# Performance work log

Measured on AMD Instinct MI355X. Metric: run time of the kernel, lower is better.

## Reference

```python
import jax, jax.numpy as jnp
import numpy as np
from jax import lax

EPS = 1e-5  # BatchNorm eps (inference-style BN with running stats)


def _bn(x, g, b, m, v):
    scale = g / jnp.sqrt(v + EPS)
    return x * scale[None, :, None, None] + (b - m * scale)[None, :, None, None]


def _conv1x1_bn(x, w, g, b, m, v):
    # ConvNormActivation(in_ch, out, k=1, activation=None) -> 1x1 conv (no bias) + BN
    y = jnp.einsum('bchw,oc->bohw', x, w)
    return _bn(y, g, b, m, v)


def _upsample_bilinear_ac(x, scale):
    # nn.Upsample(scale_factor=scale, mode='bilinear', align_corners=True)
    B, C, H, W = x.shape
    Ho, Wo = H * scale, W * scale

    def coords(n_in, n_out):
        s = jnp.arange(n_out, dtype=x.dtype) * ((n_in - 1) / (n_out - 1))
        i0 = jnp.clip(jnp.floor(s).astype(jnp.int32), 0, n_in - 2)
        t = s - i0.astype(x.dtype)
        return i0, t

    iy, ty = coords(H, Ho)
    ix, tx = coords(W, Wo)
    x = x[:, :, iy, :] * (1 - ty)[None, None, :, None] + x[:, :, iy + 1, :] * ty[None, None, :, None]
    x = x[:, :, :, ix] * (1 - tx) + x[:, :, :, ix + 1] * tx
    return x


def _dcnv2(x, off_w, off_b, w):
    # DCNv2: internal 3x3 conv -> 18 offsets (dy,dx per tap) + 9 sigmoid masks,
    # then modulated deformable 3x3 conv (stride 1, pad 1, no bias).
    B, C, H, W = x.shape
    K2 = 9
    om = lax.conv_general_dilated(x, off_w, (1, 1), ((1, 1), (1, 1)),
                                  dimension_numbers=('NCHW', 'OIHW', 'NCHW'))
    om = om + off_b[None, :, None, None]
    off = om[:, :2 * K2].reshape(B, K2, 2, H, W)          # (dy, dx) per kernel tap
    mask = jax.nn.sigmoid(om[:, 2 * K2:3 * K2])           # [B,9,H,W]

    ky, kx = jnp.meshgrid(jnp.arange(3), jnp.arange(3), indexing='ij')
    base_y = (jnp.arange(H)[None, :, None] + (ky.reshape(K2) - 1)[:, None, None]).astype(x.dtype)  # [9,H,1]
    base_x = (jnp.arange(W)[None, None, :] + (kx.reshape(K2) - 1)[:, None, None]).astype(x.dtype)  # [9,1,W]
    sy = base_y[None] + off[:, :, 0]                      # [B,9,H,W]
    sx = base_x[None] + off[:, :, 1]

    xf = x.reshape(B, C, H * W)
    y0 = jnp.floor(sy)
    x0 = jnp.floor(sx)
    val = jnp.zeros((B, C, K2, H, W), x.dtype)
    for dy in (0, 1):
        for dx in (0, 1):
            yy = y0 + dy
            xx = x0 + dx
            wgt = (1 - jnp.abs(sy - yy)) * (1 - jnp.abs(sx - xx))
            valid = (yy >= 0) & (yy <= H - 1) & (xx >= 0) & (xx <= W - 1)
            idx = jnp.clip(yy, 0, H - 1).astype(jnp.int32) * W + jnp.clip(xx, 0, W - 1).astype(jnp.int32)
            g = jnp.take_along_axis(xf, idx.reshape(B, 1, -1), axis=2).reshape(B, C, K2, H, W)
            val = val + g * (wgt * valid.astype(x.dtype))[:, None]
    val = val * mask[:, None]
    return jnp.einsum('bckhw,ock->bohw', val, w.reshape(w.shape[0], C, K2))


def _forward(f0, f1, f2, f3,
             w0, g0, b0, m0, v0, w1, g1, b1, m1, v1,
             w2, g2, b2, m2, v2, w3, g3, b3, m3, v3,
             off_w, off_b, dcn_w, gf, bf, mf, vf):
    x1 = _conv1x1_bn(f0, w0, g0, b0, m0, v0)
    x2 = _upsample_bilinear_ac(_conv1x1_bn(f1, w1, g1, b1, m1, v1), 2)
    x3 = _upsample_bilinear_ac(_conv1x1_bn(f2, w2, g2, b2, m2, v2), 4)
    x4 = _upsample_bilinear_ac(_conv1x1_bn(f3, w3, g3, b3, m3, v3), 8)
    x = jax.nn.relu(x1 + x2 + x3 + x4)
    y = _dcnv2(x, off_w, off_b, dcn_w)
    return jax.nn.relu(_bn(y, gf, bf, mf, vf))


def setup_inputs() -> dict:
    key = jax.random.key(0)
    ks = iter(jax.random.split(key, 64))

    def rn(shape, scale=1.0):
        return jax.random.normal(next(ks), shape, dtype=jnp.float32) * scale

    def ru(shape):
        return jax.random.uniform(next(ks), shape, dtype=jnp.float32)

    C = 64
    inp = {}
    inp['f0'] = rn((4, 64, 160, 160))
    inp['f1'] = rn((4, 128, 80, 80))
    inp['f2'] = rn((4, 256, 40, 40))
    inp['f3'] = rn((4, 512, 20, 20))
    for i, cin in enumerate([64, 128, 256, 512]):
        inp[f'w{i}'] = rn((C, cin), 1.0 / np.sqrt(cin))
        inp[f'g{i}'] = rn((C,))
        inp[f'b{i}'] = rn((C,))
        inp[f'm{i}'] = rn((C,))
        inp[f'v{i}'] = ru((C,))
    inp['off_w'] = rn((27, C, 3, 3), 0.01)   # small offsets, like post-training DCN
    inp['off_b'] = rn((27,), 0.01)
    inp['dcn_w'] = rn((C, C, 3, 3), 1.0 / np.sqrt(C * 9))
    inp['gf'] = rn((C,))
    inp['bf'] = rn((C,))
    inp['mf'] = rn((C,))
    inp['vf'] = ru((C,))
    return inp


def reference(f0, f1, f2, f3,
              w0, g0, b0, m0, v0, w1, g1, b1, m1, v1,
              w2, g2, b2, m2, v2, w3, g3, b3, m3, v3,
              off_w, off_b, dcn_w, gf, bf, mf, vf):
    return _forward(f0, f1, f2, f3,
                    w0, g0, b0, m0, v0, w1, g1, b1, m1, v1,
                    w2, g2, b2, m2, v2, w3, g3, b3, m3, v3,
                    off_w, off_b, dcn_w, gf, bf, mf, vf)
```

## Files before the change

kernel.cpp:

```cpp
#include <hip/hip_runtime.h>
#include <math.h>

#define EPSB 1e-5f

constexpr int B_ = 4;
constexpr int C_ = 64;
constexpr int H_ = 160;
constexpr int W_ = 160;
constexpr int HW_ = H_ * W_;

constexpr size_t X_OFF   = 0;
constexpr size_t Y1_OFF  = X_OFF  + (size_t)B_ * HW_ * 64;
constexpr size_t Y2_OFF  = Y1_OFF + (size_t)B_ * 6400 * 64;
constexpr size_t Y3_OFF  = Y2_OFF + (size_t)B_ * 1600 * 64;
constexpr size_t OM_OFF  = Y3_OFF + (size_t)B_ * 400 * 64;
constexpr size_t WR0_OFF = OM_OFF + (size_t)B_ * HW_ * 27;
constexpr size_t WTB_OFF = WR0_OFF + 4096;
constexpr size_t RWB_OFF = WTB_OFF + (9 * 64 * 72) / 2;
constexpr size_t SB_OFF  = RWB_OFF + (9 * 32 * 64) / 2;
constexpr size_t WR1_OFF = X_OFF + 0;
constexpr size_t WR2_OFF = X_OFF + 8192;
constexpr size_t WR3_OFF = X_OFF + 24576;

typedef short bf16x8 __attribute__((ext_vector_type(8)));
typedef float f32x4 __attribute__((ext_vector_type(4)));

static __device__ __forceinline__ unsigned short f2bf(float f) {
    unsigned int u = __float_as_uint(f);
    u += 0x7fff + ((u >> 16) & 1);
    return (unsigned short)(u >> 16);
}

__global__ __launch_bounds__(256) void prep_kernel(
    const float* __restrict__ g0, const float* __restrict__ b0, const float* __restrict__ m0, const float* __restrict__ v0,
    const float* __restrict__ g1, const float* __restrict__ b1, const float* __restrict__ m1, const float* __restrict__ v1,
    const float* __restrict__ g2, const float* __restrict__ b2, const float* __restrict__ m2, const float* __restrict__ v2,
    const float* __restrict__ g3, const float* __restrict__ b3, const float* __restrict__ m3, const float* __restrict__ v3,
    const float* __restrict__ gf, const float* __restrict__ bf, const float* __restrict__ mf, const float* __restrict__ vf,
    const float* __restrict__ w0, const float* __restrict__ w1, const float* __restrict__ w2, const float* __restrict__ w3,
    const float* __restrict__ dcn_w, const float* __restrict__ off_w,
    float* __restrict__ ws)
{
    int tid = blockIdx.x * 256 + threadIdx.x;
    if (tid < 320) {
        int j = tid >> 6, c = tid & 63;
        const float *g, *b, *m, *v;
        switch (j) {
            case 0: g = g0; b = b0; m = m0; v = v0; break;
            case 1: g = g1; b = b1; m = m1; v = v1; break;
            case 2: g = g2; b = b2; m = m2; v = v2; break;
            case 3: g = g3; b = b3; m = m3; v = v3; break;
            default: g = gf; b = bf; m = mf; v = vf; break;
        }
        float sc = g[c] * rsqrtf(v[c] + EPSB);
        ws[SB_OFF + j * 128 + c]      = sc;
        ws[SB_OFF + j * 128 + 64 + c] = b[c] - m[c] * sc;
        return;
    }
    int t = tid - 320;
    if (t < 4096) {
        int ci = t >> 6, o = t & 63;
        ws[WR0_OFF + t] = w0[o * 64 + ci];
        return;
    }
    t -= 4096;
    if (t < 9 * 64 * 72) {
        int k = t / 4608, r = t % 4608, o = r / 72, c = r % 72;
        float v = (c < 64) ? dcn_w[o * 576 + c * 9 + k] : 0.f;
        ((unsigned short*)(ws + WTB_OFF))[t] = f2bf(v);
        return;
    }
    t -= 9 * 64 * 72;
    if (t < 9 * 32 * 64) {
        int tap = t >> 11, r = t & 2047, o = r >> 6, ci = r & 63;
        float v = (o < 27) ? off_w[o * 576 + ci * 9 + tap] : 0.f;
        ((unsigned short*)(ws + RWB_OFF))[t] = f2bf(v);
        return;
    }
    t -= 9 * 32 * 64;
    if (t < 8192) {
        int ci = t >> 6, o = t & 63;
        ws[WR1_OFF + t] = w1[o * 128 + ci];
        return;
    }
    t -= 8192;
    if (t < 16384) {
        int ci = t >> 6, o = t & 63;
        ws[WR2_OFF + t] = w2[o * 256 + ci];
        return;
    }
    t -= 16384;
    if (t < 32768) {
        int ci = t >> 6, o = t & 63;
        ws[WR3_OFF + t] = w3[o * 512 + ci];
        return;
    }
}

__global__ __launch_bounds__(256) void conv1x1_bn_kernel(
    const float* __restrict__ f, const float* __restrict__ wr,
    const float* __restrict__ sb, float* __restrict__ out, int Cin, int hw)
{
    int xcd = blockIdx.x & 7, slot = blockIdx.x >> 3;
    int b = xcd >> 1;
    int g = (xcd & 1) * (hw >> 3) + slot;
    int o = threadIdx.x & 63;
    int p = g * 4 + (threadIdx.x >> 6);
    p = __builtin_amdgcn_readfirstlane(p);
    b = __builtin_amdgcn_readfirstlane(b);
    const float* fb = f + (size_t)b * Cin * hw + p;
    float acc = 0.f;
#pragma unroll 8
    for (int ci = 0; ci < Cin; ++ci) acc = fmaf(fb[(size_t)ci * hw], wr[ci * 64 + o], acc);
    out[((size_t)b * hw + p) * 64 + o] = fmaf(acc, sb[o], sb[64 + o]);
}

__global__ __launch_bounds__(256) void fuse_kernel(const float* __restrict__ f0, float* __restrict__ ws)
{
    __shared__ float Ot[64 * 68];

    int tid = threadIdx.x;
    int blk = blockIdx.x;
    int xcd = blk & 7, slot = blk >> 3;
    int b = xcd >> 1;
    int t = (xcd & 1) * 200 + slot;
    int p0 = t * 64;
    int lane = tid & 63;
    int cb = __builtin_amdgcn_readfirstlane(tid >> 6);
    int p = p0 + lane;
    const float* wr0 = ws + WR0_OFF + cb * 16;
    const float* sb  = ws + SB_OFF;

    {
        float acc[16];
#pragma unroll
        for (int i = 0; i < 16; i++) acc[i] = 0.f;

        const float* f0b = f0 + (size_t)b * 64 * HW_ + p;
        for (int ci0 = 0; ci0 < 64; ci0 += 8) {
            float fv[8];
#pragma unroll
            for (int j = 0; j < 8; j++) fv[j] = f0b[(size_t)(ci0 + j) * HW_];
#pragma unroll
            for (int j = 0; j < 8; j++) {
                const float* wrow = wr0 + (ci0 + j) * 64;
#pragma unroll
                for (int i = 0; i < 16; i++) acc[i] = fmaf(fv[j], wrow[i], acc[i]);
            }
        }
        float* orow = Ot + lane * 68 + cb * 16;
#pragma unroll
        for (int i = 0; i < 16; i++) {
            int o = cb * 16 + i;
            orow[i] = fmaf(acc[i], sb[o], sb[64 + o]);
        }
    }
    __syncthreads();

    {
        int chunk = lane & 15, pxo = lane >> 4;
        float* xb = ws + X_OFF + ((size_t)b * HW_ + p0) * 64;
#pragma unroll
        for (int r = 0; r < 4; r++) {
            int gpx = cb * 16 + r * 4 + pxo;
            int gp = p0 + gpx;
            int h = gp / W_, w = gp % W_;

            float fy1 = h * (79.f / 159.f); int i1 = (int)fy1; if (i1 > 78) i1 = 78; float ty1 = fy1 - i1;
            float fx1 = w * (79.f / 159.f); int j1 = (int)fx1; if (j1 > 78) j1 = 78; float tx1 = fx1 - j1;
            const float* y1 = ws + Y1_OFF + ((size_t)b * 6400 + (size_t)(i1 * 80 + j1)) * 64 + chunk * 4;
            float fy2 = h * (39.f / 159.f); int i2 = (int)fy2; if (i2 > 38) i2 = 38; float ty2 = fy2 - i2;
            float fx2 = w * (39.f / 159.f); int j2 = (int)fx2; if (j2 > 38) j2 = 38; float tx2 = fx2 - j2;
            const float* y2 = ws + Y2_OFF + ((size_t)b * 1600 + (size_t)(i2 * 40 + j2)) * 64 + chunk * 4;
            float fy3 = h * (19.f / 159.f); int i3 = (int)fy3; if (i3 > 18) i3 = 18; float ty3 = fy3 - i3;
            float fx3 = w * (19.f / 159.f); int j3 = (int)fx3; if (j3 > 18) j3 = 18; float tx3 = fx3 - j3;
            const float* y3 = ws + Y3_OFF + ((size_t)b * 400 + (size_t)(i3 * 20 + j3)) * 64 + chunk * 4;

            f32x4 A[12];
            A[0]  = *(const f32x4*)(y1);
            A[1]  = *(const f32x4*)(y1 + 64);
            A[2]  = *(const f32x4*)(y1 + 80 * 64);
            A[3]  = *(const f32x4*)(y1 + 81 * 64);
            A[4]  = *(const f32x4*)(y2);
            A[5]  = *(const f32x4*)(y2 + 64);
            A[6]  = *(const f32x4*)(y2 + 40 * 64);
            A[7]  = *(const f32x4*)(y2 + 41 * 64);
            A[8]  = *(const f32x4*)(y3);
            A[9]  = *(const f32x4*)(y3 + 64);
            A[10] = *(const f32x4*)(y3 + 20 * 64);
            A[11] = *(const f32x4*)(y3 + 21 * 64);

            f32x4 v = *(const f32x4*)(Ot + gpx * 68 + chunk * 4);

            float w00, w01, w10, w11;
            w00 = (1.f - ty1) * (1.f - tx1); w01 = (1.f - ty1) * tx1; w10 = ty1 * (1.f - tx1); w11 = ty1 * tx1;
#pragma unroll
            for (int j = 0; j < 4; j++)
                v[j] += A[0][j] * w00 + A[1][j] * w01 + A[2][j] * w10 + A[3][j] * w11;
            w00 = (1.f - ty2) * (1.f - tx2); w01 = (1.f - ty2) * tx2; w10 = ty2 * (1.f - tx2); w11 = ty2 * tx2;
#pragma unroll
            for (int j = 0; j < 4; j++)
                v[j] += A[4][j] * w00 + A[5][j] * w01 + A[6][j] * w10 + A[7][j] * w11;
            w00 = (1.f - ty3) * (1.f - tx3); w01 = (1.f - ty3) * tx3; w10 = ty3 * (1.f - tx3); w11 = ty3 * tx3;
#pragma unroll
            for (int j = 0; j < 4; j++)
                v[j] += A[8][j] * w00 + A[9][j] * w01 + A[10][j] * w10 + A[11][j] * w11;

#pragma unroll
            for (int j = 0; j < 4; j++) v[j] = fmaxf(v[j], 0.f);
            *(f32x4*)(xb + (size_t)gpx * 64 + chunk * 4) = v;
        }
    }
}

__global__ __launch_bounds__(256, 4) void dcn_fused_kernel(const float* __restrict__ off_b,
                                                           float* __restrict__ ws, float* __restrict__ out)
{
    __shared__ __align__(16) unsigned short A_lds[2][64 * 72];
    __shared__ float OMs[64 * 27];

    int tid = threadIdx.x;
    int blk = blockIdx.x;
    int xcd = blk & 7, slot = blk >> 3;
    int b = xcd >> 1;
    int t = (xcd & 1) * 200 + slot;
    int p0 = t * 64;
    int lane = tid & 63, cb = tid >> 6;
    int px = lane;
    int p = p0 + px;
    int h = p / W_, w = p % W_;
    int mrow = lane & 15, quad = lane >> 4;
    int chunk = lane & 15, pxo = lane >> 4;

    const unsigned short* rwb = (const unsigned short*)(ws + RWB_OFF);
    const unsigned short* wtb = (const unsigned short*)(ws + WTB_OFF);
    const float* xb = ws + X_OFF + (size_t)b * HW_ * 64;
    const float* sb = ws + SB_OFF + 4 * 128;

    {
        f32x4 acc2[2];
        acc2[0] = (f32x4){0.f, 0.f, 0.f, 0.f};
        acc2[1] = (f32x4){0.f, 0.f, 0.f, 0.f};

        for (int kk = 0; kk < 9; kk += 2) {
#pragma unroll
            for (int u = 0; u < 2; u++) {
                int tap = kk + u;
                if (tap > 8) break;
                int dy = tap / 3 - 1, dx = tap % 3 - 1;
                int delta = dy * W_ + dx;
                int  pss[4];
                bool vlds[4];
#pragma unroll
                for (int r = 0; r < 4; r++) {
                    int gpx = cb * 16 + r * 4 + pxo;
                    int gp = p0 + gpx;
                    int gh = gp / W_, gw = gp % W_;
                    int yy = gh + dy, xx = gw + dx;
                    vlds[r] = (yy >= 0) && (yy < H_) && (xx >= 0) && (xx < W_);
                    int ps = gp + delta;
                    pss[r] = min(max(ps, 0), HW_ - 1);
                }
                f32x4 g[4];
#pragma unroll
                for (int r = 0; r < 4; r++)
                    g[r] = *(const f32x4*)(xb + (size_t)pss[r] * 64 + chunk * 4);
#pragma unroll
                for (int r = 0; r < 4; r++) {
                    int gpx = cb * 16 + r * 4 + pxo;
                    unsigned short pk[4];
#pragma unroll
                    for (int j = 0; j < 4; j++) pk[j] = vlds[r] ? f2bf(g[r][j]) : (unsigned short)0;
                    *(unsigned int*)(A_lds[u] + gpx * 72 + chunk * 4)     = ((unsigned int)pk[1] << 16) | pk[0];
                    *(unsigned int*)(A_lds[u] + gpx * 72 + chunk * 4 + 2) = ((unsigned int)pk[3] << 16) | pk[2];
                }
            }

#pragma unroll
            for (int u = 0; u < 2; u++) {
                int tap = kk + u;
                if (tap > 8) break;
                const unsigned short* Ab = A_lds[u] + (cb * 16 + mrow) * 72;
#pragma unroll
                for (int ks = 0; ks < 2; ks++) {
                    bf16x8 af = *(const bf16x8*)(Ab + ks * 32 + quad * 8);
#pragma unroll
                    for (int nt = 0; nt < 2; nt++) {
                        bf16x8 bf_ = *(const bf16x8*)(rwb + tap * 2048 + (nt * 16 + mrow) * 64 + ks * 32 + quad * 8);
                        acc2[nt] = __builtin_amdgcn_mfma_f32_16x16x32_bf16(af, bf_, acc2[nt], 0, 0, 0);
                    }
                }
            }
        }

        __syncthreads();
        float* Cl = (float*)A_lds;
#pragma unroll
        for (int nt = 0; nt < 2; nt++) {
            int o = nt * 16 + mrow;
            if (o < 27) {
                int pr = cb * 16 + quad * 4;
#pragma unroll
                for (int r = 0; r < 4; r++) Cl[(pr + r) * 28 + o] = acc2[nt][r];
            }
        }
        __syncthreads();

        for (int k = cb; k < 9; k += 4) {
            float ady = Cl[px * 28 + 2 * k]     + off_b[2 * k];
            float adx = Cl[px * 28 + 2 * k + 1] + off_b[2 * k + 1];
            float am  = Cl[px * 28 + 18 + k]    + off_b[18 + k];
            float sy = (float)(h + k / 3 - 1) + ady;
            float sx = (float)(w + k % 3 - 1) + adx;
            float mk = 1.f / (1.f + __expf(-am));
            OMs[px * 27 + 3 * k]     = sy;
            OMs[px * 27 + 3 * k + 1] = sx;
            OMs[px * 27 + 3 * k + 2] = mk;
        }
        __syncthreads();
    }

    f32x4 acc[4];
#pragma unroll
    for (int nt = 0; nt < 4; nt++) acc[nt] = (f32x4){0.f, 0.f, 0.f, 0.f};

    for (int kk = 0; kk < 9; kk += 2) {
#pragma unroll
        for (int u = 0; u < 2; u++) {
            int k = kk + u;
            if (k > 8) break;
#pragma unroll
            for (int rp = 0; rp < 2; rp++) {
                int   idxs[2][4];
                float wvs[2][4];
#pragma unroll
                for (int rr = 0; rr < 2; rr++) {
                    int r = rp * 2 + rr;
                    int gpx = cb * 16 + r * 4 + pxo;
                    float sy = OMs[gpx * 27 + 3 * k];
                    float sx = OMs[gpx * 27 + 3 * k + 1];
                    float mk = OMs[gpx * 27 + 3 * k + 2];
                    float y0f = floorf(sy), x0f = floorf(sx);
                    int y0 = (int)y0f, x0 = (int)x0f;
                    float ty = sy - y0f, tx = sx - x0f;
#pragma unroll
                    for (int cr = 0; cr < 4; cr++) {
                        int dy = cr >> 1, dx = cr & 1;
                        int yy = y0 + dy, xx = x0 + dx;
                        float wy = dy ? ty : 1.f - ty;
                        float wx = dx ? tx : 1.f - tx;
                        bool vld = (yy >= 0) && (yy < H_) && (xx >= 0) && (xx < W_);
                        int yc = min(max(yy, 0), H_ - 1);
                        int xc = min(max(xx, 0), W_ - 1);
                        idxs[rr][cr] = yc * W_ + xc;
                        wvs[rr][cr]  = vld ? wy * wx * mk : 0.f;
                    }
                }
                f32x4 g[2][4];
#pragma unroll
                for (int rr = 0; rr < 2; rr++)
#pragma unroll
                    for (int cr = 0; cr < 4; cr++)
                        g[rr][cr] = *(const f32x4*)(xb + (size_t)idxs[rr][cr] * 64 + chunk * 4);
#pragma unroll
                for (int rr = 0; rr < 2; rr++) {
                    int r = rp * 2 + rr;
                    int gpx = cb * 16 + r * 4 + pxo;
                    f32x4 v = (f32x4){0.f, 0.f, 0.f, 0.f};
#pragma unroll
                    for (int cr = 0; cr < 4; cr++) {
                        float wv = wvs[rr][cr];
#pragma unroll
                        for (int j = 0; j < 4; j++) v[j] = fmaf(g[rr][cr][j], wv, v[j]);
                    }
                    unsigned short pk[4];
#pragma unroll
                    for (int j = 0; j < 4; j++) pk[j] = f2bf(v[j]);
                    *(unsigned int*)(A_lds[u] + gpx * 72 + chunk * 4)     = ((unsigned int)pk[1] << 16) | pk[0];
                    *(unsigned int*)(A_lds[u] + gpx * 72 + chunk * 4 + 2) = ((unsigned int)pk[3] << 16) | pk[2];
                }
            }
        }

#pragma unroll
        for (int u = 0; u < 2; u++) {
            int k = kk + u;
            if (k > 8) break;
            const unsigned short* Ab = A_lds[u] + (cb * 16 + mrow) * 72;
#pragma unroll
            for (int ks = 0; ks < 2; ks++) {
                bf16x8 af = *(const bf16x8*)(Ab + ks * 32 + quad * 8);
#pragma unroll
                for (int nt = 0; nt < 4; nt++) {
                    bf16x8 bf_ = *(const bf16x8*)(wtb + k * 4608 + (nt * 16 + mrow) * 72 + ks * 32 + quad * 8);
                    acc[nt] = __builtin_amdgcn_mfma_f32_16x16x32_bf16(af, bf_, acc[nt], 0, 0, 0);
                }
            }
        }
    }

    __syncthreads();
    float* C_lds = (float*)A_lds;
#pragma unroll
    for (int nt = 0; nt < 4; nt++) {
        int o = nt * 16 + mrow;
        int pxb = cb * 16 + quad * 4;
#pragma unroll
        for (int r = 0; r < 4; r++) C_lds[o * 65 + pxb + r] = acc[nt][r];
    }
    __syncthreads();
#pragma unroll
    for (int i = 0; i < 16; i++) {
        int o = cb * 16 + i;
        float v = C_lds[o * 65 + lane];
        v = fmaf(v, sb[o], sb[64 + o]);
        out[((size_t)b * 64 + o) * HW_ + p0 + lane] = fmaxf(v, 0.f);
    }
}

extern "C" void kernel_launch(void* const* d_in, const int* in_sizes, int n_in,
                              void* d_out, int out_size, void* d_ws, size_t ws_size,
                              hipStream_t stream)
{
    const float* f0 = (const float*)d_in[0];
    const float* f1 = (const float*)d_in[1];
    const float* f2 = (const float*)d_in[2];
    const float* f3 = (const float*)d_in[3];
    const float* w0 = (const float*)d_in[4];
    const float* g0 = (const float*)d_in[5];
    const float* b0 = (const float*)d_in[6];
    const float* m0 = (const float*)d_in[7];
    const float* v0 = (const float*)d_in[8];
    const float* w1 = (const float*)d_in[9];
    const float* g1 = (const float*)d_in[10];
    const float* b1 = (const float*)d_in[11];
    const float* m1 = (const float*)d_in[12];
    const float* v1 = (const float*)d_in[13];
    const float* w2 = (const float*)d_in[14];
    const float* g2 = (const float*)d_in[15];
    const float* b2 = (const float*)d_in[16];
    const float* m2 = (const float*)d_in[17];
    const float* v2 = (const float*)d_in[18];
    const float* w3 = (const float*)d_in[19];
    const float* g3 = (const float*)d_in[20];
    const float* b3 = (const float*)d_in[21];
    const float* m3 = (const float*)d_in[22];
    const float* v3 = (const float*)d_in[23];
    const float* off_w = (const float*)d_in[24];
    const float* off_b = (const float*)d_in[25];
    const float* dcn_w = (const float*)d_in[26];
    const float* gf = (const float*)d_in[27];
    const float* bf = (const float*)d_in[28];
    const float* mf = (const float*)d_in[29];
    const float* vf = (const float*)d_in[30];

    float* ws  = (float*)d_ws;
    float* out = (float*)d_out;

    prep_kernel<<<dim3(476), dim3(256), 0, stream>>>(
        g0, b0, m0, v0, g1, b1, m1, v1, g2, b2, m2, v2, g3, b3, m3, v3,
        gf, bf, mf, vf, w0, w1, w2, w3, dcn_w, off_w, ws);

    conv1x1_bn_kernel<<<dim3(6400), dim3(256), 0, stream>>>(f1, ws + WR1_OFF, ws + SB_OFF + 128, ws + Y1_OFF, 128, 6400);
    conv1x1_bn_kernel<<<dim3(1600), dim3(256), 0, stream>>>(f2, ws + WR2_OFF, ws + SB_OFF + 256, ws + Y2_OFF, 256, 1600);
    conv1x1_bn_kernel<<<dim3(400),  dim3(256), 0, stream>>>(f3, ws + WR3_OFF, ws + SB_OFF + 384, ws + Y3_OFF, 512, 400);

    fuse_kernel<<<dim3(1600), dim3(256), 0, stream>>>(f0, ws);

    dcn_fused_kernel<<<dim3(1600), dim3(256), 0, stream>>>(off_b, ws, out);
}
```

Baseline: 338.6 us.

## Merge three 1x1 conv launches into one register-tiled kernel with split-K reduction

Result: faster. 297.8 us (-12.0%).

```diff
diff --git a/kernel.cpp b/kernel.cpp
--- a/kernel.cpp
+++ b/kernel.cpp
@@ -97,22 +97,89 @@
     }
 }
 
-__global__ __launch_bounds__(256) void conv1x1_bn_kernel(
-    const float* __restrict__ f, const float* __restrict__ wr,
-    const float* __restrict__ sb, float* __restrict__ out, int Cin, int hw)
+__global__ __launch_bounds__(256) void conv_all_kernel(
+    const float* __restrict__ f1in, const float* __restrict__ f2in, const float* __restrict__ f3in,
+    float* __restrict__ ws)
 {
-    int xcd = blockIdx.x & 7, slot = blockIdx.x >> 3;
-    int b = xcd >> 1;
-    int g = (xcd & 1) * (hw >> 3) + slot;
-    int o = threadIdx.x & 63;
-    int p = g * 4 + (threadIdx.x >> 6);
-    p = __builtin_amdgcn_readfirstlane(p);
-    b = __builtin_amdgcn_readfirstlane(b);
-    const float* fb = f + (size_t)b * Cin * hw + p;
-    float acc = 0.f;
-#pragma unroll 8
-    for (int ci = 0; ci < Cin; ++ci) acc = fmaf(fb[(size_t)ci * hw], wr[ci * 64 + o], acc);
-    out[((size_t)b * hw + p) * 64 + o] = fmaf(acc, sb[o], sb[64 + o]);
+    __shared__ float R0[64 * 65];
+    __shared__ float R1[64 * 65];
+    __shared__ float SBl[128];
+
+    int blk = blockIdx.x;
+    const float* fin; const float* wr; const float* sbg; float* yout;
+    int Cin, hw, tile;
+    if (blk < 400)      { fin = f1in; wr = ws + WR1_OFF; sbg = ws + SB_OFF + 128; yout = ws + Y1_OFF; Cin = 128; hw = 6400; tile = blk; }
+    else if (blk < 500) { fin = f2in; wr = ws + WR2_OFF; sbg = ws + SB_OFF + 256; yout = ws + Y2_OFF; Cin = 256; hw = 1600; tile = blk - 400; }
+    else                { fin = f3in; wr = ws + WR3_OFF; sbg = ws + SB_OFF + 384; yout = ws + Y3_OFF; Cin = 512; hw = 400;  tile = blk - 500; }
+
+    int tid  = threadIdx.x;
+    int lane = tid & 63;
+    int wv   = __builtin_amdgcn_readfirstlane(tid >> 6);
+
+    if (tid < 128) SBl[tid] = sbg[tid];
+
+    int P = tile * 64 + lane;
+    int b = P / hw;
+    int p = P - b * hw;
+
+    int cq = Cin >> 2;
+    const float* fb = fin + ((size_t)b * Cin + (size_t)wv * cq) * hw + p;
+    const float* wq = wr + (wv * cq) * 64;
+
+    float acc[64];
+#pragma unroll
+    for (int o = 0; o < 64; o++) acc[o] = 0.f;
+
+    for (int c0 = 0; c0 < cq; c0 += 8) {
+        float fv[8];
+#pragma unroll
+        for (int j = 0; j < 8; j++) fv[j] = fb[(size_t)(c0 + j) * hw];
+#pragma unroll
+        for (int j = 0; j < 8; j++) {
+            const float* wrow = wq + (c0 + j) * 64;
+#pragma unroll
+            for (int o = 0; o < 64; o++) acc[o] = fmaf(fv[j], wrow[o], acc[o]);
+        }
+    }
+
+    if (wv == 2) {
+#pragma unroll
+        for (int o = 0; o < 64; o++) R0[lane * 65 + o] = acc[o];
+    }
+    if (wv == 3) {
+#pragma unroll
+        for (int o = 0; o < 64; o++) R1[lane * 65 + o] = acc[o];
+    }
+    __syncthreads();
+    if (wv == 0) {
+#pragma unroll
+        for (int o = 0; o < 64; o++) acc[o] += R0[lane * 65 + o];
+    }
+    if (wv == 1) {
+#pragma unroll
+        for (int o = 0; o < 64; o++) acc[o] += R1[lane * 65 + o];
+    }
+    __syncthreads();
+    if (wv == 1) {
+#pragma unroll
+        for (int o = 0; o < 64; o++) R0[lane * 65 + o] = acc[o];
+    }
+    __syncthreads();
+    if (wv == 0) {
+#pragma unroll
+        for (int o = 0; o < 64; o++) {
+            float v = acc[o] + R0[lane * 65 + o];
+            R1[lane * 65 + o] = fmaf(v, SBl[o], SBl[64 + o]);
+        }
+    }
+    __syncthreads();
+
+#pragma unroll
+    for (int it = 0; it < 16; it++) {
+        int idx = it * 256 + tid;
+        int px = idx >> 6, o = idx & 63;
+        yout[(size_t)(tile * 64 + px) * 64 + o] = R1[px * 65 + o];
+    }
 }
 
 __global__ __launch_bounds__(256) void fuse_kernel(const float* __restrict__ f0, float* __restrict__ ws)
@@ -461,9 +528,7 @@
         g0, b0, m0, v0, g1, b1, m1, v1, g2, b2, m2, v2, g3, b3, m3, v3,
         gf, bf, mf, vf, w0, w1, w2, w3, dcn_w, off_w, ws);
 
-    conv1x1_bn_kernel<<<dim3(6400), dim3(256), 0, stream>>>(f1, ws + WR1_OFF, ws + SB_OFF + 128, ws + Y1_OFF, 128, 6400);
-    conv1x1_bn_kernel<<<dim3(1600), dim3(256), 0, stream>>>(f2, ws + WR2_OFF, ws + SB_OFF + 256, ws + Y2_OFF, 256, 1600);
-    conv1x1_bn_kernel<<<dim3(400),  dim3(256), 0, stream>>>(f3, ws + WR3_OFF, ws + SB_OFF + 384, ws + Y3_OFF, 512, 400);
+    conv_all_kernel<<<dim3(525), dim3(256), 0, stream>>>(f1, f2, f3, ws);
 
     fuse_kernel<<<dim3(1600), dim3(256), 0, stream>>>(f0, ws);
 
```
